# Kernel optimization log

Measured on AMD Instinct MI355X. Metric: run time of the kernel, lower is better.

The kernel has to match this reference:

```python
import jax, jax.numpy as jnp
import numpy as np

MAX_DISP = 20  # matches init_kwargs max_displacement


def setup_inputs() -> dict:
    key = jax.random.key(0)
    k1, k2 = jax.random.split(key)
    feat1 = jax.random.normal(k1, (4, 128, 64, 64), dtype=jnp.float32)
    feat2 = jax.random.normal(k2, (4, 128, 64, 64), dtype=jnp.float32)
    return {"feat1": feat1, "feat2": feat2}


def reference(feat1, feat2):
    pad = MAX_DISP
    D = 2 * pad + 1  # displacement window side (41)
    b, c, h, w = feat1.shape
    feat2_pad = jnp.pad(feat2, ((0, 0), (0, 0), (pad, pad), (pad, pad)))

    def step(carry, ij):
        i = ij // D
        j = ij % D
        sl = jax.lax.dynamic_slice(feat2_pad, (0, 0, i, j), (b, c, h, w))
        # dot over channel dim -> [b, h, w]
        return carry, jnp.sum(feat1 * sl, axis=1)

    # scan over all D*D displacements keeps peak memory at one [b,c,h,w] slice
    _, corr = jax.lax.scan(step, None, jnp.arange(D * D))  # [D*D, b, h, w]
    return jnp.transpose(corr, (1, 0, 2, 3))  # [b, D*D, h, w]
```

## Files before the change

kernel.cpp:

```cpp
#include <hip/hip_runtime.h>
#include <stdint.h>


#define NB 4
#define NC 128
#define NH 64
#define NW 64
#define PAD 20
#define ND 41
#define HW (NH * NW)
#define ROW_U4 1024

typedef __attribute__((ext_vector_type(8))) __bf16 bf16x8;
typedef __attribute__((ext_vector_type(16))) float f32x16;

__device__ __forceinline__ unsigned int pk2(float a, float b) {
  unsigned short lo = __builtin_bit_cast(unsigned short, (__bf16)a);
  unsigned short hi = __builtin_bit_cast(unsigned short, (__bf16)b);
  return (unsigned int)lo | ((unsigned int)hi << 16);
}

__global__ __launch_bounds__(256) void conv_kernel(
    const float* __restrict__ f1, const float* __restrict__ f2,
    uint4* __restrict__ ws) {
  const int blk = blockIdx.x;
  const int isF2 = blk >> 9;
  const int by = (blk >> 1) & 255;
  const int chalf = blk & 1;
  const int b = by >> 6, y = by & 63;
  const float* src = (isF2 ? f2 : f1) + (size_t)b * NC * HW + (size_t)y * NW;
  uint4* dst = ws + (size_t)isF2 * (NB * NH * ROW_U4) + (size_t)by * ROW_U4;
  const int x = threadIdx.x & 63;
  const int cq = threadIdx.x >> 6;
#pragma unroll
  for (int it = 0; it < 2; ++it) {
    const int cg = chalf * 8 + it * 4 + cq;
    float v[8];
#pragma unroll
    for (int i = 0; i < 8; ++i) v[i] = src[(size_t)(cg * 8 + i) * HW + x];
    uint4 u;
    u.x = pk2(v[0], v[1]);
    u.y = pk2(v[2], v[3]);
    u.z = pk2(v[4], v[5]);
    u.w = pk2(v[6], v[7]);
    dst[cg * 64 + x] = u;
  }
}

__global__ __launch_bounds__(256, 4) void corr_main(
    const uint4* __restrict__ ws, float* __restrict__ out) {
  __shared__ float cbuf[2][64 * 64];

  const int bid = blockIdx.x;
  const int lid = (bid & 7) * 128 + (bid >> 3);
  const int dq = lid & 3;
  const int y = (lid >> 2) & 63;
  const int b = lid >> 8;

  const int t = threadIdx.x;
  const int lane = t & 63;
  const int wv = t >> 6;
  const int I = wv & 1;
  const int J = wv >> 1;
  const int kh = lane >> 5;

  const int xa = I * 32 + (lane & 31);
  const int xb = J * 32 + (lane & 31);
  const int col = (lane & 31) + 32 * J;
  const int rbase = kh * 4 + I * 32;
  const int xg = t & 63;
  const int g = t >> 6;

  const uint4* f1t = ws;
  const uint4* f2t = ws + NB * NH * ROW_U4;

  const int dBeg = (ND * dq) / 4;
  const int dEnd = (ND * (dq + 1)) / 4;
  int a0 = 20 - y;
  if (a0 < dBeg) a0 = dBeg;
  if (a0 > dEnd) a0 = dEnd;
  int a1 = 84 - y;
  if (a1 < a0) a1 = a0;
  if (a1 > dEnd) a1 = dEnd;

  const size_t outBase = (size_t)b * (ND * ND) * HW + (size_t)y * NW;

  for (int di = dBeg; di < a0; ++di) {
    const size_t dB = outBase + (size_t)di * ND * HW;
    for (int k = g; k < ND; k += 4) out[dB + (size_t)k * HW + xg] = 0.f;
  }
  for (int di = a1; di < dEnd; ++di) {
    const size_t dB = outBase + (size_t)di * ND * HW;
    for (int k = g; k < ND; k += 4) out[dB + (size_t)k * HW + xg] = 0.f;
  }
  const int n = a1 - a0;
  if (n <= 0) return;

  const uint4* f1row = f1t + (size_t)(b * 64 + y) * ROW_U4 + kh * 64 + xb;
  bf16x8 bfrag[8];
#pragma unroll
  for (int ks = 0; ks < 8; ++ks)
    bfrag[ks] = __builtin_bit_cast(bf16x8, f1row[ks * 128]);

  const uint4* f2row = f2t + (size_t)(b * 64) * ROW_U4 + kh * 64 + xa;

  int p = 0;
#pragma unroll 1
  for (int j = 0; j < n; ++j) {
    const int yp = y + (a0 + j) - PAD;
    const uint4* ap = f2row + (size_t)yp * ROW_U4;
    uint4 a[8];
#pragma unroll
    for (int ks = 0; ks < 8; ++ks) a[ks] = ap[ks * 128];

    if (j > 0) {
      const size_t dB = outBase + (size_t)(a0 + j - 1) * ND * HW;
      const float* cb = cbuf[p ^ 1];
      for (int k = g; k < ND; k += 4) {
        const int xs = xg + k - PAD;
        const float vv = (xs >= 0 && xs < NW) ? cb[xs * 64 + xg] : 0.f;
        out[dB + (size_t)k * HW + xg] = vv;
      }
    }

    f32x16 acc;
#pragma unroll
    for (int r = 0; r < 16; ++r) acc[r] = 0.f;
#pragma unroll
    for (int ks = 0; ks < 8; ++ks)
      acc = __builtin_amdgcn_mfma_f32_32x32x16_bf16(
          __builtin_bit_cast(bf16x8, a[ks]), bfrag[ks], acc, 0, 0, 0);
#pragma unroll
    for (int r = 0; r < 16; ++r) {
      const int row = rbase + (r & 3) + 8 * (r >> 2);
      cbuf[p][row * 64 + col] = acc[r];
    }
    __syncthreads();
    p ^= 1;
  }

  {
    const size_t dB = outBase + (size_t)(a0 + n - 1) * ND * HW;
    const float* cb = cbuf[p ^ 1];
    for (int k = g; k < ND; k += 4) {
      const int xs = xg + k - PAD;
      const float vv = (xs >= 0 && xs < NW) ? cb[xs * 64 + xg] : 0.f;
      out[dB + (size_t)k * HW + xg] = vv;
    }
  }
}

__device__ __forceinline__ float f4elem(const float4 v, int j) {
  return j == 0 ? v.x : j == 1 ? v.y : j == 2 ? v.z : v.w;
}

__device__ __forceinline__ void convwrite(const float4 (&v)[8],
                                          uint4* __restrict__ lds, int xq,
                                          int cg) {
#pragma unroll
  for (int j = 0; j < 4; ++j) {
    const int x = xq * 4 + j;
    uint4 u;
    u.x = pk2(f4elem(v[0], j), f4elem(v[1], j));
    u.y = pk2(f4elem(v[2], j), f4elem(v[3], j));
    u.z = pk2(f4elem(v[4], j), f4elem(v[5], j));
    u.w = pk2(f4elem(v[6], j), f4elem(v[7], j));
    lds[x * 16 + (cg ^ (x & 7))] = u;
  }
}

__global__ __launch_bounds__(256, 2) void corr_fallback(
    const float* __restrict__ feat1, const float* __restrict__ feat2,
    float* __restrict__ out) {
  __shared__ uint4 f2s[2][64 * 16];
  __shared__ float cbuf[2][64 * 64];

  const int bid = blockIdx.x;
  const int lid = (bid & 7) * 64 + (bid >> 3);
  const int half = lid & 1;
  const int y = (lid >> 1) & 63;
  const int b = lid >> 7;

  const int t = threadIdx.x;
  const int lane = t & 63;
  const int wv = t >> 6;
  const int I = wv & 1;
  const int J = wv >> 1;
  const int xa = I * 32 + (lane & 31);
  const int xb = J * 32 + (lane & 31);
  const int kh = lane >> 5;
  const int aBase = xa * 16, aSw = xa & 7;
  const int bBase = xb * 16, bSw = xb & 7;
  const int col = (lane & 31) + J * 32;
  const int rbase = kh * 4 + I * 32;
  const int xg = t & 63;
  const int g = t >> 6;
  const int xq = t & 15;
  const int cg = t >> 4;
  const size_t rowoff = (size_t)cg * 8 * HW + xq * 4;
  const float* f1row = feat1 + (size_t)b * NC * HW + (size_t)y * NW + rowoff;
  const float* f2row0 = feat2 + (size_t)b * NC * HW + rowoff;
  const size_t outBase = ((size_t)b * (ND * ND) * NH + y) * NW;

  int dBeg, dEnd;
  if (half == 0) {
    dBeg = (y < PAD) ? (PAD - y) : 0;
    dEnd = PAD + 1;
  } else {
    dBeg = PAD + 1;
    const int e = (NH + PAD) - y;
    dEnd = e < ND ? e : ND;
  }
  const int zBeg = half ? dEnd : 0;
  const int zEnd = half ? ND : dBeg;
  for (int di = zBeg; di < zEnd; ++di) {
    const size_t dB = outBase + (size_t)di * ND * HW;
    for (int k = g; k < ND; k += 4) out[dB + (size_t)k * HW + xg] = 0.f;
  }
  if (dBeg >= dEnd) return;

  float4 v[8];
#pragma unroll
  for (int i = 0; i < 8; ++i) v[i] = *(const float4*)(f1row + (size_t)i * HW);
  uint4* f1tmp = (uint4*)&cbuf[0][0];
  convwrite(v, f1tmp, xq, cg);
  {
    const int yp0 = y + dBeg - PAD;
#pragma unroll
    for (int i = 0; i < 8; ++i)
      v[i] = *(const float4*)(f2row0 + (size_t)yp0 * NW + (size_t)i * HW);
  }
  __syncthreads();
  bf16x8 bfrag[8];
#pragma unroll
  for (int ks = 0; ks < 8; ++ks) {
    const int q = ks * 2 + kh;
    bfrag[ks] = __builtin_bit_cast(bf16x8, f1tmp[bBase + (q ^ bSw)]);
  }
  __syncthreads();

  const int nIter = dEnd - dBeg;
  int p = 0;
#pragma unroll 1
  for (int j = 0; j < nIter; ++j) {
    convwrite(v, f2s[p], xq, cg);
    {
      const int nj = (j + 1 < nIter) ? j + 1 : j;
      const int ypn = y + dBeg + nj - PAD;
#pragma unroll
      for (int i = 0; i < 8; ++i)
        v[i] = *(const float4*)(f2row0 + (size_t)ypn * NW + (size_t)i * HW);
    }
    __syncthreads();

    f32x16 acc;
#pragma unroll
    for (int r = 0; r < 16; ++r) acc[r] = 0.f;
#pragma unroll
    for (int ks = 0; ks < 8; ++ks) {
      const int q = ks * 2 + kh;
      bf16x8 aa = __builtin_bit_cast(bf16x8, f2s[p][aBase + (q ^ aSw)]);
      acc = __builtin_amdgcn_mfma_f32_32x32x16_bf16(aa, bfrag[ks], acc, 0, 0, 0);
    }
#pragma unroll
    for (int r = 0; r < 16; ++r) {
      const int row = rbase + (r & 3) + 8 * (r >> 2);
      cbuf[p][row * 64 + col] = acc[r];
    }
    if (j > 0) {
      const size_t dBase = outBase + (size_t)(dBeg + j - 1) * ND * HW;
      const float* cb = cbuf[p ^ 1];
      for (int k = g; k < ND; k += 4) {
        const int xs = xg + k - PAD;
        const float vv = (xs >= 0 && xs < NW) ? cb[xs * 64 + xg] : 0.f;
        out[dBase + (size_t)k * HW + xg] = vv;
      }
    }
    p ^= 1;
  }
  __syncthreads();
  {
    const size_t dBase = outBase + (size_t)(dEnd - 1) * ND * HW;
    const float* cb = cbuf[p ^ 1];
    for (int k = g; k < ND; k += 4) {
      const int xs = xg + k - PAD;
      const float vv = (xs >= 0 && xs < NW) ? cb[xs * 64 + xg] : 0.f;
      out[dBase + (size_t)k * HW + xg] = vv;
    }
  }
}

extern "C" void kernel_launch(void* const* d_in, const int* in_sizes, int n_in,
                              void* d_out, int out_size, void* d_ws,
                              size_t ws_size, hipStream_t stream) {
  (void)in_sizes; (void)n_in; (void)out_size;
  const float* f1 = (const float*)d_in[0];
  const float* f2 = (const float*)d_in[1];
  float* out = (float*)d_out;
  const size_t need = (size_t)2 * NB * NH * ROW_U4 * sizeof(uint4);
  if (ws_size >= need && d_ws != nullptr) {
    uint4* ws = (uint4*)d_ws;
    conv_kernel<<<dim3(1024), dim3(256), 0, stream>>>(f1, f2, ws);
    corr_main<<<dim3(NB * NH * 4), dim3(256), 0, stream>>>(ws, out);
  } else {
    corr_fallback<<<dim3(NB * NH * 2), dim3(256), 0, stream>>>(f1, f2, out);
  }
}
```

Baseline: 39.54 us.

## Repartition correlation blocks by vertical displacement and four-row groups with vectorized stores

Each block of the correlation kernel now handles one (batch, vertical displacement) pair over four consecutive output rows, instead of one output row over a quarter of the displacements. Results are staged in a shared diagonal buffer so every block writes 256 contiguous floats per displacement with 16-byte nontemporal stores, rather than scattered 64-float row writes. The grid grows to 2624 blocks and the launch-bounds occupancy hint drops from 4 to 2. In exchange the f1 row is reloaded for every displacement, there are two barriers per row, and blocks whose rows fall outside the image now run the zero-fill through the same staging path.

```diff
diff --git a/kernel.cpp b/kernel.cpp
--- a/kernel.cpp
+++ b/kernel.cpp
@@ -13,6 +13,7 @@
 
 typedef __attribute__((ext_vector_type(8))) __bf16 bf16x8;
 typedef __attribute__((ext_vector_type(16))) float f32x16;
+typedef __attribute__((ext_vector_type(4))) float f32x4;
 
 __device__ __forceinline__ unsigned int pk2(float a, float b) {
   unsigned short lo = __builtin_bit_cast(unsigned short, (__bf16)a);
@@ -47,15 +48,18 @@
   }
 }
 
-__global__ __launch_bounds__(256, 4) void corr_main(
+__global__ __launch_bounds__(256, 2) void corr_main(
     const uint4* __restrict__ ws, float* __restrict__ out) {
-  __shared__ float cbuf[2][64 * 64];
-
-  const int bid = blockIdx.x;
-  const int lid = (bid & 7) * 128 + (bid >> 3);
-  const int dq = lid & 3;
-  const int y = (lid >> 2) & 63;
-  const int b = lid >> 8;
+  __shared__ float diag[ND * 4 * 64];
+  __shared__ float cbuf[64 * 64];
+
+  const int raw = blockIdx.x;
+  const int lid = (raw & 7) * 328 + (raw >> 3);
+  const int y4 = lid & 15;
+  const int g2 = lid >> 4;
+  const int di = g2 % ND;
+  const int b = g2 / ND;
+  const int y0 = y4 * 4;
 
   const int t = threadIdx.x;
   const int lane = t & 63;
@@ -74,79 +78,52 @@
   const uint4* f1t = ws;
   const uint4* f2t = ws + NB * NH * ROW_U4;
 
-  const int dBeg = (ND * dq) / 4;
-  const int dEnd = (ND * (dq + 1)) / 4;
-  int a0 = 20 - y;
-  if (a0 < dBeg) a0 = dBeg;
-  if (a0 > dEnd) a0 = dEnd;
-  int a1 = 84 - y;
-  if (a1 < a0) a1 = a0;
-  if (a1 > dEnd) a1 = dEnd;
-
-  const size_t outBase = (size_t)b * (ND * ND) * HW + (size_t)y * NW;
-
-  for (int di = dBeg; di < a0; ++di) {
-    const size_t dB = outBase + (size_t)di * ND * HW;
-    for (int k = g; k < ND; k += 4) out[dB + (size_t)k * HW + xg] = 0.f;
-  }
-  for (int di = a1; di < dEnd; ++di) {
-    const size_t dB = outBase + (size_t)di * ND * HW;
-    for (int k = g; k < ND; k += 4) out[dB + (size_t)k * HW + xg] = 0.f;
-  }
-  const int n = a1 - a0;
-  if (n <= 0) return;
-
-  const uint4* f1row = f1t + (size_t)(b * 64 + y) * ROW_U4 + kh * 64 + xb;
-  bf16x8 bfrag[8];
-#pragma unroll
-  for (int ks = 0; ks < 8; ++ks)
-    bfrag[ks] = __builtin_bit_cast(bf16x8, f1row[ks * 128]);
-
-  const uint4* f2row = f2t + (size_t)(b * 64) * ROW_U4 + kh * 64 + xa;
-
-  int p = 0;
 #pragma unroll 1
-  for (int j = 0; j < n; ++j) {
-    const int yp = y + (a0 + j) - PAD;
-    const uint4* ap = f2row + (size_t)yp * ROW_U4;
-    uint4 a[8];
-#pragma unroll
-    for (int ks = 0; ks < 8; ++ks) a[ks] = ap[ks * 128];
-
-    if (j > 0) {
-      const size_t dB = outBase + (size_t)(a0 + j - 1) * ND * HW;
-      const float* cb = cbuf[p ^ 1];
-      for (int k = g; k < ND; k += 4) {
-        const int xs = xg + k - PAD;
-        const float vv = (xs >= 0 && xs < NW) ? cb[xs * 64 + xg] : 0.f;
-        out[dB + (size_t)k * HW + xg] = vv;
+  for (int yy = 0; yy < 4; ++yy) {
+    const int y = y0 + yy;
+    const int yp = y + di - PAD;
+    const bool vld = (yp >= 0 && yp < NH);
+
+    if (vld) {
+      const uint4* ap = f2t + (size_t)(b * 64 + yp) * ROW_U4 + kh * 64 + xa;
+      const uint4* bp = f1t + (size_t)(b * 64 + y) * ROW_U4 + kh * 64 + xb;
+      uint4 a[8], bb[8];
+#pragma unroll
+      for (int ks = 0; ks < 8; ++ks) {
+        a[ks] = ap[ks * 128];
+        bb[ks] = bp[ks * 128];
       }
-    }
-
-    f32x16 acc;
-#pragma unroll
-    for (int r = 0; r < 16; ++r) acc[r] = 0.f;
-#pragma unroll
-    for (int ks = 0; ks < 8; ++ks)
-      acc = __builtin_amdgcn_mfma_f32_32x32x16_bf16(
-          __builtin_bit_cast(bf16x8, a[ks]), bfrag[ks], acc, 0, 0, 0);
-#pragma unroll
-    for (int r = 0; r < 16; ++r) {
-      const int row = rbase + (r & 3) + 8 * (r >> 2);
-      cbuf[p][row * 64 + col] = acc[r];
+      f32x16 acc;
+#pragma unroll
+      for (int r = 0; r < 16; ++r) acc[r] = 0.f;
+#pragma unroll
+      for (int ks = 0; ks < 8; ++ks)
+        acc = __builtin_amdgcn_mfma_f32_32x32x16_bf16(
+            __builtin_bit_cast(bf16x8, a[ks]),
+            __builtin_bit_cast(bf16x8, bb[ks]), acc, 0, 0, 0);
+#pragma unroll
+      for (int r = 0; r < 16; ++r) {
+        const int row = rbase + (r & 3) + 8 * (r >> 2);
+        cbuf[row * 64 + col] = acc[r];
+      }
     }
     __syncthreads();
-    p ^= 1;
-  }
-
-  {
-    const size_t dB = outBase + (size_t)(a0 + n - 1) * ND * HW;
-    const float* cb = cbuf[p ^ 1];
+
     for (int k = g; k < ND; k += 4) {
       const int xs = xg + k - PAD;
-      const float vv = (xs >= 0 && xs < NW) ? cb[xs * 64 + xg] : 0.f;
-      out[dB + (size_t)k * HW + xg] = vv;
-    }
+      const float vv =
+          (vld && xs >= 0 && xs < NW) ? cbuf[xs * 64 + xg] : 0.f;
+      diag[(k * 4 + yy) * 64 + xg] = vv;
+    }
+    __syncthreads();
+  }
+
+  const size_t pBase =
+      ((size_t)(b * (ND * ND) + di * ND) * NH + y0) * NW;
+  for (int k = g; k < ND; k += 4) {
+    const f32x4 vv = *(const f32x4*)&diag[k * 256 + lane * 4];
+    __builtin_nontemporal_store(
+        vv, (f32x4*)(out + pBase + (size_t)k * HW + lane * 4));
   }
 }
 
@@ -301,7 +278,7 @@
   if (ws_size >= need && d_ws != nullptr) {
     uint4* ws = (uint4*)d_ws;
     conv_kernel<<<dim3(1024), dim3(256), 0, stream>>>(f1, f2, ws);
-    corr_main<<<dim3(NB * NH * 4), dim3(256), 0, stream>>>(ws, out);
+    corr_main<<<dim3(NB * ND * 16), dim3(256), 0, stream>>>(ws, out);
   } else {
     corr_fallback<<<dim3(NB * NH * 2), dim3(256), 0, stream>>>(f1, f2, out);
   }
```

After: 54.90 us. 38.9% more time.
